# Kernel tuning notes

Hardware: AMD Instinct MI355X
Metric: run time of the kernel (lower is better)

## Reference

```python
import jax, jax.numpy as jnp
from jax import lax
import numpy as np


def _bn(x, g, b, eps=1e-5):
    # BatchNorm2d in training mode: biased batch stats over (N,H,W) per channel
    m = jnp.mean(x, axis=(0, 2, 3), keepdims=True)
    v = jnp.mean((x - m) ** 2, axis=(0, 2, 3), keepdims=True)
    return (x - m) * lax.rsqrt(v + eps) * g[None, :, None, None] + b[None, :, None, None]


def _conv(x, w, b, pad):
    y = lax.conv_general_dilated(x, w, (1, 1), [(pad, pad), (pad, pad)],
                                 dimension_numbers=('NCHW', 'OIHW', 'NCHW'))
    return y + b[None, :, None, None]


def _prelu(x, a):
    return jnp.where(x >= 0, x, a * x)


def _maxpool2(x):
    return lax.reduce_window(x, -jnp.inf, lax.max, (1, 1, 2, 2), (1, 1, 2, 2), 'VALID')


def _up2(x):
    # UpsamplingBilinear2d(scale_factor=2) -> bilinear, align_corners=True
    B, C, H, W = x.shape
    def idx(n):
        pos = jnp.arange(2 * n, dtype=x.dtype) * (n - 1) / (2 * n - 1)
        lo = jnp.floor(pos).astype(jnp.int32)
        hi = jnp.minimum(lo + 1, n - 1)
        return lo, hi, pos - lo.astype(x.dtype)
    lo, hi, f = idx(H)
    x = x[:, :, lo, :] * (1 - f)[:, None] + x[:, :, hi, :] * f[:, None]
    lo, hi, f = idx(W)
    x = x[:, :, :, lo] * (1 - f) + x[:, :, :, hi] * f
    return x


def _forward(x, n16, sigma16, bias16, prelu_a,
             bn3_g, bn3_b, bn32_g, bn32_b, bn64_g, bn64_b, bn128_g, bn128_b,
             w1, b1, w2, b2, w3, b3, w4, b4, w5, b5, w6, b6, w7, b7, w11, b11):
    B, C, H, W = x.shape
    # 16 enhancement curves fused: r_k = x^{n_k} / (x^{n_k} + sigma_k^{n_k} + bias_k)
    xn = x[None] ** n16[:, None, None, None, None]          # (16,B,3,H,W)
    r = xn / (xn + (sigma16 ** n16)[:, None, None, None, None]
              + bias16[:, None, None, None, None])
    # each branch gets its own BatchNorm2d(3) stats (same affine params)
    r = jax.vmap(lambda t: _bn(t, bn3_g, bn3_b))(r)
    x_fusion = jnp.transpose(r, (1, 0, 2, 3, 4)).reshape(B, 16 * C, H, W)
    x1 = _bn(_maxpool2(_prelu(_conv(x_fusion, w1, b1, 1), prelu_a)), bn32_g, bn32_b)
    x2 = _bn(_maxpool2(_prelu(_conv(x1, w2, b2, 1), prelu_a)), bn64_g, bn64_b)
    x3 = _bn(_maxpool2(_prelu(_conv(x2, w3, b3, 1), prelu_a)), bn128_g, bn128_b)
    x4 = _bn(_conv(x3, w4, b4, 1), bn128_g, bn128_b)
    x5 = _bn(_up2(_prelu(_conv(jnp.concatenate([x4, x3], 1), w5, b5, 1), prelu_a)), bn64_g, bn64_b)
    x6 = _bn(_up2(_prelu(_conv(jnp.concatenate([x2, x5], 1), w6, b6, 1), prelu_a)), bn32_g, bn32_b)
    x_out = jax.nn.sigmoid(_up2(_prelu(_conv(jnp.concatenate([x1, x6], 1), w7, b7, 1), prelu_a)))
    x_out = _conv(x_out, w11, b11, 0)
    x_mean = jnp.mean(x, axis=1, keepdims=True)
    x_out1 = jnp.mean(x_out, axis=1, keepdims=True)
    return x_out1 * (x / (x_mean + 1e-6))


def setup_inputs() -> dict:
    key = jax.random.key(0)
    ks = jax.random.split(key, 16)
    B, H, W = 8, 256, 256
    nf = 32
    x = jax.random.uniform(ks[0], (B, 3, H, W), jnp.float32, 1e-3, 1.0)
    n16 = jnp.arange(1, 17, dtype=jnp.float32) * 0.5
    sigma16 = jnp.full((16,), 0.5, jnp.float32)
    bias16 = jnp.full((16,), 1e-4, jnp.float32)
    prelu_a = jnp.float32(0.25)
    def cw(k, o, i, kk):
        return jax.random.normal(k, (o, i, kk, kk), jnp.float32) * 0.05
    def cb(o):
        return jnp.zeros((o,), jnp.float32)
    return dict(
        x=x, n16=n16, sigma16=sigma16, bias16=bias16, prelu_a=prelu_a,
        bn3_g=jnp.ones((3,), jnp.float32), bn3_b=jnp.zeros((3,), jnp.float32),
        bn32_g=jnp.ones((32,), jnp.float32), bn32_b=jnp.zeros((32,), jnp.float32),
        bn64_g=jnp.ones((64,), jnp.float32), bn64_b=jnp.zeros((64,), jnp.float32),
        bn128_g=jnp.ones((128,), jnp.float32), bn128_b=jnp.zeros((128,), jnp.float32),
        w1=cw(ks[1], nf, 48, 3), b1=cb(nf),
        w2=cw(ks[2], 2 * nf, nf, 3), b2=cb(2 * nf),
        w3=cw(ks[3], 4 * nf, 2 * nf, 3), b3=cb(4 * nf),
        w4=cw(ks[4], 4 * nf, 4 * nf, 3), b4=cb(4 * nf),
        w5=cw(ks[5], 2 * nf, 8 * nf, 3), b5=cb(2 * nf),
        w6=cw(ks[6], nf, 4 * nf, 3), b6=cb(nf),
        w7=cw(ks[7], nf, 2 * nf, 3), b7=cb(nf),
        w11=cw(ks[8], 3, nf, 1), b11=cb(3),
    )


def reference(x, n16, sigma16, bias16, prelu_a,
              bn3_g, bn3_b, bn32_g, bn32_b, bn64_g, bn64_b, bn128_g, bn128_b,
              w1, b1, w2, b2, w3, b3, w4, b4, w5, b5, w6, b6, w7, b7, w11, b11):
    return _forward(x, n16, sigma16, bias16, prelu_a,
                    bn3_g, bn3_b, bn32_g, bn32_b, bn64_g, bn64_b, bn128_g, bn128_b,
                    w1, b1, w2, b2, w3, b3, w4, b4, w5, b5, w6, b6, w7, b7, w11, b11)
```

## Files before the change

### kernel.cpp

```cpp
#include <hip/hip_runtime.h>

#define FAST_EXP2(x) __builtin_amdgcn_exp2f(x)
#define FAST_LOG2(x) __builtin_amdgcn_logf(x)
#define FAST_RCP(x)  __builtin_amdgcn_rcpf(x)

static constexpr size_t S3_SUM=0,   S3_SQ=48;
static constexpr size_t S32A_SUM=96,  S32A_SQ=128;
static constexpr size_t S64A_SUM=160, S64A_SQ=224;
static constexpr size_t S128A_SUM=288,S128A_SQ=416;
static constexpr size_t S128B_SUM=544,S128B_SQ=672;
static constexpr size_t S64B_SUM=800, S64B_SQ=864;
static constexpr size_t S32B_SUM=928, S32B_SQ=960;
static constexpr size_t SPB_=2016, WBAR_=2032, BBAR_=2064;
static constexpr size_t T1_=4096;
static constexpr size_t T2_=T1_+4194304;
static constexpr size_t T3_=T2_+2097152;
static constexpr size_t T4_=T3_+1048576;
static constexpr size_t C5_=T4_+1048576;
static constexpr size_t U5_=C5_+524288;
static constexpr size_t C6_=U5_+2097152;
static constexpr size_t U6_=C6_+1048576;
static constexpr size_t C7_=U6_+4194304;
static constexpr size_t W1S_=C7_+4194304;
static constexpr size_t B1S_=W1S_+13824;
static constexpr size_t PAD_=B1S_+64;

__device__ inline void bn_ab(const float* __restrict__ sum, const float* __restrict__ sq,
                             const float* __restrict__ g, const float* __restrict__ bb,
                             float invN, int c, float& a, float& b)
{
    float m   = sum[c]*invN;
    float var = fmaxf(sq[c]*invN - m*m, 0.f);
    float inv = rsqrtf(var + 1e-5f);
    a = g[c]*inv;
    b = bb[c] - m*a;
}

__global__ __launch_bounds__(256) void k_branch_stats(
    const float* __restrict__ x, const float* __restrict__ n16,
    const float* __restrict__ sig16, const float* __restrict__ b16,
    float* __restrict__ sum, float* __restrict__ sq)
{
    const int c = blockIdx.x >> 6;
    const int chunk = blockIdx.x & 63;
    float nk[16], den[16];
#pragma unroll
    for (int k = 0; k < 16; ++k) { nk[k] = n16[k]; den[k] = powf(sig16[k], nk[k]) + b16[k]; }
    float s[16], q[16];
#pragma unroll
    for (int k = 0; k < 16; ++k) { s[k] = 0.f; q[k] = 0.f; }
    const int per = 8192;
    int start = chunk * per;
    for (int i = start + (int)threadIdx.x; i < start + per; i += 256) {
        int b = i >> 16, hw = i & 65535;
        float xv = x[(size_t)(b*3 + c)*65536 + hw];
        float t = FAST_LOG2(xv);
#pragma unroll
        for (int k = 0; k < 16; ++k) {
            float v = FAST_EXP2(nk[k]*t);
            float r = v * FAST_RCP(v + den[k]);
            s[k] += r; q[k] += r*r;
        }
    }
    __shared__ float red[4][32];
    int lane = threadIdx.x & 63, wid = threadIdx.x >> 6;
#pragma unroll
    for (int k = 0; k < 16; ++k) {
#pragma unroll
        for (int off = 32; off > 0; off >>= 1) {
            s[k] += __shfl_down(s[k], off);
            q[k] += __shfl_down(q[k], off);
        }
    }
    if (lane == 0) {
#pragma unroll
        for (int k = 0; k < 16; ++k) { red[wid][k] = s[k]; red[wid][16+k] = q[k]; }
    }
    __syncthreads();
    if (threadIdx.x < 32) {
        float v = red[0][threadIdx.x] + red[1][threadIdx.x] + red[2][threadIdx.x] + red[3][threadIdx.x];
        int k = threadIdx.x & 15;
        if (threadIdx.x < 16) atomicAdd(&sum[k*3 + c], v);
        else                  atomicAdd(&sq[k*3 + c], v);
    }
}

__global__ __launch_bounds__(256) void k_stats(
    const float* __restrict__ in, int C, int HW, int nchunks, int per,
    float* __restrict__ sum, float* __restrict__ sq)
{
    int c = blockIdx.x / nchunks;
    int chunk = blockIdx.x - c*nchunks;
    float s = 0.f, q = 0.f;
    int start = chunk * per, end = start + per;
    for (int i = start + (int)threadIdx.x; i < end; i += 256) {
        int b = i / HW, hw = i - b*HW;
        float v = in[((size_t)b*C + c)*HW + hw];
        s += v; q += v*v;
    }
#pragma unroll
    for (int off = 32; off > 0; off >>= 1) { s += __shfl_down(s, off); q += __shfl_down(q, off); }
    __shared__ float ss[4], qq[4];
    int lane = threadIdx.x & 63, wid = threadIdx.x >> 6;
    if (lane == 0) { ss[wid] = s; qq[wid] = q; }
    __syncthreads();
    if (threadIdx.x == 0) {
        atomicAdd(&sum[c], ss[0]+ss[1]+ss[2]+ss[3]);
        atomicAdd(&sq[c],  qq[0]+qq[1]+qq[2]+qq[3]);
    }
}

__global__ __launch_bounds__(256) void k_fill(
    float* __restrict__ out, const float* __restrict__ bias, int C, int HW, int total)
{
    int idx = blockIdx.x*256 + threadIdx.x;
    if (idx < total) {
        int c = (idx / HW) % C;
        out[idx] = bias[c];
    }
}

__global__ __launch_bounds__(256) void k_prep_all(
    const float* __restrict__ s3sum, const float* __restrict__ s3sq,
    const float* __restrict__ bn3_g, const float* __restrict__ bn3_b,
    const float* __restrict__ n16, const float* __restrict__ sig16, const float* __restrict__ b16,
    const float* __restrict__ w11, const float* __restrict__ b11,
    const float* __restrict__ w1, const float* __restrict__ b1,
    float* __restrict__ w1s, float* __restrict__ b1s, float* __restrict__ padg,
    float* __restrict__ spb, float* __restrict__ wbar, float* __restrict__ bbar)
{
    __shared__ float a3[48], b3[48];
    int tid = threadIdx.x;
    if (tid < 48) {
        float m   = s3sum[tid]*(1.f/524288.f);
        float var = fmaxf(s3sq[tid]*(1.f/524288.f) - m*m, 0.f);
        float inv = rsqrtf(var + 1e-5f);
        float a   = bn3_g[tid % 3]*inv;
        a3[tid] = a;
        b3[tid] = bn3_b[tid % 3] - m*a;
    }
    if (tid < 16) spb[tid] = powf(sig16[tid], n16[tid]) + b16[tid];
    else if (tid >= 64 && tid < 96) { int j = tid - 64; wbar[j] = (w11[j] + w11[32+j] + w11[64+j]) * (1.f/3.f); }
    else if (tid == 96) bbar[0] = (b11[0] + b11[1] + b11[2]) * (1.f/3.f);
    __syncthreads();
    if (tid < 48) padg[tid] = -b3[tid] * FAST_RCP(a3[tid]);
    for (int t = tid; t < 13824; t += 256) {
        int ci = (t / 9) % 48;
        w1s[t] = w1[t] * a3[ci];
    }
    if (tid < 32) {
        float s = b1[tid];
        const float* wp = w1 + tid*432;
        for (int i = 0; i < 432; ++i) s += wp[i] * b3[i/9];
        b1s[tid] = s;
    }
}

template<int COG>
__device__ inline void stats_reduce8(float (&ssum)[COG], float (&ssq)[COG],
                                     float (*redst)[16], int cob,
                                     float* __restrict__ gsum, float* __restrict__ gsq)
{
    int lane = threadIdx.x & 63, wid = threadIdx.x >> 6;
#pragma unroll
    for (int co = 0; co < COG; ++co) {
#pragma unroll
        for (int off = 32; off > 0; off >>= 1) {
            ssum[co] += __shfl_down(ssum[co], off);
            ssq[co]  += __shfl_down(ssq[co],  off);
        }
    }
    if (lane == 0) {
#pragma unroll
        for (int co = 0; co < COG; ++co) { redst[wid][co] = ssum[co]; redst[wid][8+co] = ssq[co]; }
    }
    __syncthreads();
    if (threadIdx.x < 16) {
        float v = redst[0][threadIdx.x] + redst[1][threadIdx.x] + redst[2][threadIdx.x] + redst[3][threadIdx.x];
        if (threadIdx.x < 8) atomicAdd(&gsum[cob + threadIdx.x], v);
        else                 atomicAdd(&gsq[cob + threadIdx.x - 8], v);
    }
}

template<int COG>
__global__ __launch_bounds__(256,2) void k_conv1f(
    const float* __restrict__ x,
    const float* __restrict__ n16, const float* __restrict__ spb,
    const float* __restrict__ w1s, const float* __restrict__ b1s,
    const float* __restrict__ padg,
    const float* __restrict__ prelu_a,
    float* __restrict__ out, float* __restrict__ gsum, float* __restrict__ gsq)
{
    const int tx = threadIdx.x & 15, ty = threadIdx.x >> 4;
    const int nco = 32 / COG;
    const int b = blockIdx.z / nco, cob = (blockIdx.z - b*nco)*COG;
    const int x0 = blockIdx.x*32, y0 = blockIdx.y*32;

    __shared__ float wl[COG*48*9];
    __shared__ float rl[2][3*1224];
    __shared__ float nl16[16], dl16[16], padl[48];
    __shared__ float redst[4][16];

    for (int t = threadIdx.x; t < COG*48*9; t += 256) {
        int co = t % COG; int rest = t / COG;
        int kk = rest % 9; int ci = rest / 9;
        wl[t] = w1s[(((size_t)(cob+co))*48 + ci)*9 + kk];
    }
    if (threadIdx.x < 16)       nl16[threadIdx.x]    = n16[threadIdx.x];
    else if (threadIdx.x < 32)  dl16[threadIdx.x-16] = spb[threadIdx.x-16];
    else if (threadIdx.x < 80)  padl[threadIdx.x-32] = padg[threadIdx.x-32];

    float tlr[14];
    int off_[14]; int chpack = 0; int okf = 0;
#pragma unroll
    for (int j = 0; j < 14; ++j) {
        int i = threadIdx.x + 256*j;
        if (i < 3468) {
            int ch = i / 1156, jj = i - ch*1156;
            int rr = jj / 34, cc = jj - rr*34;
            int gy = y0 - 1 + rr, gx = x0 - 1 + cc;
            bool ok = (unsigned)gy < 256u && (unsigned)gx < 256u;
            off_[j] = ch*1224 + rr*36 + cc;
            chpack |= ch << (2*j);
            tlr[j] = 0.f;
            if (ok) {
                okf |= 1 << j;
                tlr[j] = FAST_LOG2(x[((size_t)(b*3+ch))*65536 + gy*256 + gx]);
            }
        } else { off_[j] = 3671; tlr[j] = 0.f; }
    }

    float acc[COG][4];
#pragma unroll
    for (int i = 0; i < COG; ++i)
#pragma unroll
        for (int j = 0; j < 4; ++j) acc[i][j] = 0.f;

    {
        float nk = nl16[0], dk = dl16[0];
#pragma unroll
        for (int j = 0; j < 14; ++j) {
            int ch = (chpack >> (2*j)) & 3;
            float pv = padl[ch];
            float v = FAST_EXP2(nk * tlr[j]);
            float rv = v * FAST_RCP(v + dk);
            rl[0][off_[j]] = ((okf >> j) & 1) ? rv : pv;
        }
    }
    __syncthreads();

#pragma unroll 1
    for (int k = 0; k < 16; ++k) {
        if (k < 15) {
            float nk = nl16[k+1], dk = dl16[k+1];
#pragma unroll
            for (int j = 0; j < 14; ++j) {
                int ch = (chpack >> (2*j)) & 3;
                float pv = padl[(k+1)*3 + ch];
                float v = FAST_EXP2(nk * tlr[j]);
                float rv = v * FAST_RCP(v + dk);
                rl[(k+1)&1][off_[j]] = ((okf >> j) & 1) ? rv : pv;
            }
        }
        const float* rbuf = rl[k&1];
#pragma unroll
        for (int ch = 0; ch < 3; ++ch) {
            const float* tlp = rbuf + ch*1224 + (2*ty)*36 + 2*tx;
            float iv[4][4];
#pragma unroll
            for (int r = 0; r < 4; ++r) {
                float2 a2 = *(const float2*)(tlp + r*36);
                float2 b2 = *(const float2*)(tlp + r*36 + 2);
                iv[r][0]=a2.x; iv[r][1]=a2.y; iv[r][2]=b2.x; iv[r][3]=b2.y;
            }
            const float* wbase = &wl[((k*3+ch)*9)*COG];
#pragma unroll
            for (int kh = 0; kh < 3; ++kh)
#pragma unroll
            for (int kw = 0; kw < 3; ++kw) {
                const int kk = kh*3 + kw;
                float wv[COG];
#pragma unroll
                for (int q = 0; q < COG/4; ++q) {
                    float4 wq = *((const float4*)(wbase + kk*COG) + q);
                    wv[4*q+0]=wq.x; wv[4*q+1]=wq.y; wv[4*q+2]=wq.z; wv[4*q+3]=wq.w;
                }
#pragma unroll
                for (int co = 0; co < COG; ++co)
#pragma unroll
                    for (int py = 0; py < 2; ++py)
#pragma unroll
                        for (int px = 0; px < 2; ++px)
                            acc[co][py*2+px] += wv[co]*iv[py+kh][px+kw];
            }
        }
        __syncthreads();
    }

    float a = __ldg(prelu_a);
    int pyp = (y0 >> 1) + ty, pxp = (x0 >> 1) + tx;
    float ssum[COG], ssq[COG];
#pragma unroll
    for (int co = 0; co < COG; ++co) {
        float bv = b1s[cob + co];
        float v0 = acc[co][0] + bv, v1 = acc[co][1] + bv;
        float v2 = acc[co][2] + bv, v3 = acc[co][3] + bv;
        v0 = v0 >= 0.f ? v0 : a*v0; v1 = v1 >= 0.f ? v1 : a*v1;
        v2 = v2 >= 0.f ? v2 : a*v2; v3 = v3 >= 0.f ? v3 : a*v3;
        float m = fmaxf(fmaxf(v0,v1), fmaxf(v2,v3));
        out[(((size_t)b*32 + cob + co)*128 + pyp)*128 + pxp] = m;
        ssum[co] = m; ssq[co] = m*m;
    }
    __syncthreads();
    stats_reduce8<COG>(ssum, ssq, redst, cob, gsum, gsq);
}

template<int COG, bool POOL>
__global__ __launch_bounds__(256,2) void k_conv_big(
    const float* __restrict__ in1, int C1,
    const float* __restrict__ sum1, const float* __restrict__ sq1,
    const float* __restrict__ g1, const float* __restrict__ bb1, float invN1,
    const float* __restrict__ w, const float* __restrict__ bias,
    int Cout, int H, int W, const float* __restrict__ prelu_a, int do_prelu,
    float* __restrict__ out, float* __restrict__ gsum, float* __restrict__ gsq)
{
    const int Cin = C1;
    const int tx = threadIdx.x & 15, ty = threadIdx.x >> 4;
    const int nco = Cout / COG;
    const int b = blockIdx.z / nco, cob = (blockIdx.z - b*nco)*COG;
    const int x0 = blockIdx.x*64, y0 = blockIdx.y*32;

    __shared__ float wl[COG*64*9];
    __shared__ float tile[2][34*68];
    __shared__ float redst[4][16];

    for (int t = threadIdx.x; t < COG*Cin*9; t += 256) {
        int co = t % COG; int rest = t / COG;
        int k = rest % 9; int ci = rest / 9;
        wl[t] = w[(((size_t)(cob+co))*Cin + ci)*9 + k];
    }

    float acc[COG][8];
#pragma unroll
    for (int i = 0; i < COG; ++i)
#pragma unroll
        for (int j = 0; j < 8; ++j) acc[i][j] = 0.f;

#pragma unroll 1
    for (int cb = 0; cb < Cin; cb += 2) {
#pragma unroll
        for (int sub = 0; sub < 2; ++sub) {
            int ci = cb + sub;
            float scv = 1.f, shv = 0.f;
            if (sum1) bn_ab(sum1, sq1, g1, bb1, invN1, ci, scv, shv);
            const float* base = in1 + ((size_t)b*Cin + ci)*H*W;
#pragma unroll 1
            for (int i = threadIdx.x; i < 34*66; i += 256) {
                int r = i / 66, c = i - r*66;
                int gy = y0 - 1 + r, gx = x0 - 1 + c;
                float v = 0.f;
                if ((unsigned)gy < (unsigned)H && (unsigned)gx < (unsigned)W)
                    v = base[(size_t)gy*W + gx]*scv + shv;
                tile[sub][r*68 + c] = v;
            }
        }
        __syncthreads();
#pragma unroll
        for (int sub = 0; sub < 2; ++sub) {
            const float* tl = &tile[sub][(2*ty)*68 + 4*tx];
            float iv[4][6];
#pragma unroll
            for (int r = 0; r < 4; ++r) {
                float4 av = *(const float4*)(tl + r*68);
                float2 bv = *(const float2*)(tl + r*68 + 4);
                iv[r][0]=av.x; iv[r][1]=av.y; iv[r][2]=av.z; iv[r][3]=av.w;
                iv[r][4]=bv.x; iv[r][5]=bv.y;
            }
            const float* wbase = &wl[(cb+sub)*9*COG];
#pragma unroll
            for (int kh = 0; kh < 3; ++kh)
#pragma unroll
            for (int kw = 0; kw < 3; ++kw) {
                const int k = kh*3 + kw;
                float wv[COG];
#pragma unroll
                for (int q = 0; q < COG/4; ++q) {
                    float4 wq = *((const float4*)(wbase + k*COG) + q);
                    wv[4*q+0]=wq.x; wv[4*q+1]=wq.y; wv[4*q+2]=wq.z; wv[4*q+3]=wq.w;
                }
#pragma unroll
                for (int co = 0; co < COG; ++co)
#pragma unroll
                    for (int py = 0; py < 2; ++py)
#pragma unroll
                        for (int px = 0; px < 4; ++px)
                            acc[co][py*4+px] += wv[co]*iv[py+kh][px+kw];
            }
        }
        __syncthreads();
    }

    float a = __ldg(prelu_a);
    float ssum[COG], ssq[COG];
    if (POOL) {
        const int Hp = H >> 1, Wp = W >> 1;
        int pyp = (y0 >> 1) + ty, pxp = (x0 >> 1) + 2*tx;
#pragma unroll
        for (int co = 0; co < COG; ++co) {
            float bv = bias[cob + co];
            float v[8];
#pragma unroll
            for (int p = 0; p < 8; ++p) {
                float t = acc[co][p] + bv;
                v[p] = t >= 0.f ? t : a*t;
            }
            float2 st;
            st.x = fmaxf(fmaxf(v[0], v[1]), fmaxf(v[4], v[5]));
            st.y = fmaxf(fmaxf(v[2], v[3]), fmaxf(v[6], v[7]));
            *(float2*)(out + (((size_t)b*Cout + cob + co)*Hp + pyp)*Wp + pxp) = st;
            ssum[co] = st.x + st.y; ssq[co] = st.x*st.x + st.y*st.y;
        }
        stats_reduce8<COG>(ssum, ssq, redst, cob, gsum, gsq);
    } else {
        int oy = y0 + 2*ty, ox = x0 + 4*tx;
#pragma unroll
        for (int co = 0; co < COG; ++co) {
            float bv = bias[cob + co];
            float* op = out + (((size_t)b*Cout + cob + co)*H + oy)*W + ox;
#pragma unroll
            for (int py = 0; py < 2; ++py) {
                float4 st;
                float t0 = acc[co][py*4+0] + bv, t1 = acc[co][py*4+1] + bv;
                float t2 = acc[co][py*4+2] + bv, t3 = acc[co][py*4+3] + bv;
                if (do_prelu) {
                    t0 = t0 >= 0.f ? t0 : a*t0; t1 = t1 >= 0.f ? t1 : a*t1;
                    t2 = t2 >= 0.f ? t2 : a*t2; t3 = t3 >= 0.f ? t3 : a*t3;
                }
                st.x=t0; st.y=t1; st.z=t2; st.w=t3;
                *(float4*)(op + py*W) = st;
            }
        }
    }
}

template<int COG, int MAXCI, bool POOL, bool SPLIT, bool STATS>
__global__ __launch_bounds__(256,4) void k_conv32(
    const float* __restrict__ in1, int C1,
    const float* __restrict__ sum1, const float* __restrict__ sq1,
    const float* __restrict__ g1, const float* __restrict__ bb1, float invN1,
    const float* __restrict__ in2, int C2,
    const float* __restrict__ sum2, const float* __restrict__ sq2,
    const float* __restrict__ g2, const float* __restrict__ bb2, float invN2,
    const float* __restrict__ w, const float* __restrict__ bias,
    int Cout, int H, int W, const float* __restrict__ prelu_a, int do_prelu,
    int ciN, int nsplit,
    float* __restrict__ out, float* __restrict__ gsum, float* __restrict__ gsq)
{
    const int Cin = C1 + C2;
    const int tx = threadIdx.x & 15, ty = threadIdx.x >> 4;
    const int nco = Cout / COG;
    int z = blockIdx.z;
    const int sp = z % nsplit; z /= nsplit;
    const int b = z / nco, cob = (z - b*nco)*COG;
    const int ci0 = sp * ciN;
    const int x0 = blockIdx.x*32, y0 = blockIdx.y*32;

    __shared__ float wl[COG*MAXCI*9];
    __shared__ float tile[2][34*36];
    __shared__ float redst[4][16];

    for (int t = threadIdx.x; t < COG*ciN*9; t += 256) {
        int co = t % COG; int rest = t / COG;
        int k = rest % 9; int ci = rest / 9;
        wl[t] = w[(((size_t)(cob+co))*Cin + ci0 + ci)*9 + k];
    }

    float acc[COG][4];
#pragma unroll
    for (int i = 0; i < COG; ++i)
#pragma unroll
        for (int j = 0; j < 4; ++j) acc[i][j] = 0.f;

#pragma unroll 1
    for (int cb = 0; cb < ciN; cb += 2) {
#pragma unroll
        for (int sub = 0; sub < 2; ++sub) {
            int ci = ci0 + cb + sub;
            const float* in; int cc; int Cn;
            const float* sm; const float* sqp; const float* gg; const float* bbp; float iN;
            if (ci < C1) { in = in1; cc = ci;      Cn = C1; sm = sum1; sqp = sq1; gg = g1; bbp = bb1; iN = invN1; }
            else         { in = in2; cc = ci - C1; Cn = C2; sm = sum2; sqp = sq2; gg = g2; bbp = bb2; iN = invN2; }
            float scv = 1.f, shv = 0.f;
            if (sm) bn_ab(sm, sqp, gg, bbp, iN, cc, scv, shv);
            const float* base = in + ((size_t)b*Cn + cc)*H*W;
#pragma unroll 1
            for (int i = threadIdx.x; i < 34*34; i += 256) {
                int r = i / 34, c = i - r*34;
                int gy = y0 - 1 + r, gx = x0 - 1 + c;
                float v = 0.f;
                if ((unsigned)gy < (unsigned)H && (unsigned)gx < (unsigned)W)
                    v = base[(size_t)gy*W + gx]*scv + shv;
                tile[sub][r*36 + c] = v;
            }
        }
        __syncthreads();
#pragma unroll
        for (int sub = 0; sub < 2; ++sub) {
            const float* tl = &tile[sub][(2*ty)*36 + 2*tx];
            float iv[4][4];
#pragma unroll
            for (int r = 0; r < 4; ++r) {
                float2 a2 = *(const float2*)(tl + r*36);
                float2 b2 = *(const float2*)(tl + r*36 + 2);
                iv[r][0]=a2.x; iv[r][1]=a2.y; iv[r][2]=b2.x; iv[r][3]=b2.y;
            }
            const float* wbase = &wl[(cb+sub)*9*COG];
#pragma unroll
            for (int kh = 0; kh < 3; ++kh)
#pragma unroll
            for (int kw = 0; kw < 3; ++kw) {
                const int k = kh*3 + kw;
                float wv[COG];
#pragma unroll
                for (int q = 0; q < COG/4; ++q) {
                    float4 wq = *((const float4*)(wbase + k*COG) + q);
                    wv[4*q+0]=wq.x; wv[4*q+1]=wq.y; wv[4*q+2]=wq.z; wv[4*q+3]=wq.w;
                }
#pragma unroll
                for (int co = 0; co < COG; ++co)
#pragma unroll
                    for (int py = 0; py < 2; ++py)
#pragma unroll
                        for (int px = 0; px < 2; ++px)
                            acc[co][py*2+px] += wv[co]*iv[py+kh][px+kw];
            }
        }
        __syncthreads();
    }

    if (SPLIT) {
        int oy = y0 + 2*ty, ox = x0 + 2*tx;
#pragma unroll
        for (int co = 0; co < COG; ++co) {
            float* op = out + (((size_t)b*Cout + cob + co)*H + oy)*W + ox;
            atomicAdd(&op[0],     acc[co][0]);
            atomicAdd(&op[1],     acc[co][1]);
            atomicAdd(&op[W],     acc[co][2]);
            atomicAdd(&op[W + 1], acc[co][3]);
        }
    } else {
        float a = __ldg(prelu_a);
        float ssum[COG], ssq[COG];
        if (POOL) {
            const int Hp = H >> 1, Wp = W >> 1;
            int pyp = (y0 >> 1) + ty, pxp = (x0 >> 1) + tx;
#pragma unroll
            for (int co = 0; co < COG; ++co) {
                float bv = bias[cob + co];
                float v0 = acc[co][0] + bv, v1 = acc[co][1] + bv;
                float v2 = acc[co][2] + bv, v3 = acc[co][3] + bv;
                v0 = v0 >= 0.f ? v0 : a*v0; v1 = v1 >= 0.f ? v1 : a*v1;
                v2 = v2 >= 0.f ? v2 : a*v2; v3 = v3 >= 0.f ? v3 : a*v3;
                float m = fmaxf(fmaxf(v0,v1), fmaxf(v2,v3));
                out[(((size_t)b*Cout + cob + co)*Hp + pyp)*Wp + pxp] = m;
                ssum[co] = m; ssq[co] = m*m;
            }
            if (STATS) stats_reduce8<COG>(ssum, ssq, redst, cob, gsum, gsq);
        } else {
            int oy = y0 + 2*ty, ox = x0 + 2*tx;
#pragma unroll
            for (int co = 0; co < COG; ++co) {
                float bv = bias[cob + co];
                float* op = out + (((size_t)b*Cout + cob + co)*H + oy)*W + ox;
                float v0 = acc[co][0] + bv, v1 = acc[co][1] + bv;
                float v2 = acc[co][2] + bv, v3 = acc[co][3] + bv;
                if (do_prelu) {
                    v0 = v0 >= 0.f ? v0 : a*v0; v1 = v1 >= 0.f ? v1 : a*v1;
                    v2 = v2 >= 0.f ? v2 : a*v2; v3 = v3 >= 0.f ? v3 : a*v3;
                }
                op[0] = v0; op[1] = v1; op[W] = v2; op[W+1] = v3;
                ssum[co] = v0+v1+v2+v3; ssq[co] = v0*v0+v1*v1+v2*v2+v3*v3;
            }
            if (STATS) stats_reduce8<COG>(ssum, ssq, redst, cob, gsum, gsq);
        }
    }
}

__global__ __launch_bounds__(256) void k_up2(
    const float* __restrict__ in, float* __restrict__ out, int C, int h, int w,
    const float* __restrict__ prelu_a, int do_prelu,
    float* __restrict__ gsum, float* __restrict__ gsq)
{
    int idx = blockIdx.x*256 + threadIdx.x;
    int W2 = 2*w, H2 = 2*h;
    float a = do_prelu ? __ldg(prelu_a) : 0.f;
    int ox = idx % W2; int t = idx / W2; int oy = t % H2; int bc = t / H2;
    float py = ((float)oy * (float)(h-1)) / (float)(2*h - 1);
    int ly = (int)floorf(py); int hy = min(ly+1, h-1); float fy = py - (float)ly;
    float px = ((float)ox * (float)(w-1)) / (float)(2*w - 1);
    int lx = (int)floorf(px); int hx = min(lx+1, w-1); float fx = px - (float)lx;
    const float* p = in + (size_t)bc*h*w;
    float v00 = p[(size_t)ly*w + lx], v01 = p[(size_t)ly*w + hx];
    float v10 = p[(size_t)hy*w + lx], v11 = p[(size_t)hy*w + hx];
    if (do_prelu) {
        v00 = v00 >= 0.f ? v00 : a*v00;
        v01 = v01 >= 0.f ? v01 : a*v01;
        v10 = v10 >= 0.f ? v10 : a*v10;
        v11 = v11 >= 0.f ? v11 : a*v11;
    }
    float v0 = v00*(1.f-fx) + v01*fx;
    float v1 = v10*(1.f-fx) + v11*fx;
    float v = v0*(1.f-fy) + v1*fy;
    out[idx] = v;
    float s = v, q = v*v;
#pragma unroll
    for (int off = 32; off > 0; off >>= 1) { s += __shfl_down(s, off); q += __shfl_down(q, off); }
    __shared__ float ss[4], qq[4];
    int lane = threadIdx.x & 63, wid = threadIdx.x >> 6;
    if (lane == 0) { ss[wid] = s; qq[wid] = q; }
    __syncthreads();
    if (threadIdx.x == 0) {
        int c = bc % C;
        atomicAdd(&gsum[c], ss[0]+ss[1]+ss[2]+ss[3]);
        atomicAdd(&gsq[c],  qq[0]+qq[1]+qq[2]+qq[3]);
    }
}

__global__ __launch_bounds__(256) void k_final(
    const float* __restrict__ c7, const float* __restrict__ x,
    const float* __restrict__ wbar, const float* __restrict__ bbar,
    float* __restrict__ out)
{
    int idx = blockIdx.x*256 + threadIdx.x;
    if (idx >= 8*65536) return;
    int hw = idx & 65535, b = idx >> 16;
    int oy = hw >> 8, ox = hw & 255;
    float py = ((float)oy * 127.f) / 255.f;
    int ly = (int)floorf(py); int hy = min(ly+1, 127); float fy = py - (float)ly;
    float px = ((float)ox * 127.f) / 255.f;
    int lx = (int)floorf(px); int hx = min(lx+1, 127); float fx = px - (float)lx;
    float w00 = (1.f-fy)*(1.f-fx), w01 = (1.f-fy)*fx, w10 = fy*(1.f-fx), w11v = fy*fx;
    const float* base = c7 + (size_t)b*32*16384;
    float accum = bbar[0];
#pragma unroll 8
    for (int j = 0; j < 32; ++j) {
        const float* p = base + (size_t)j*16384;
        float v = p[ly*128 + lx]*w00 + p[ly*128 + hx]*w01 + p[hy*128 + lx]*w10 + p[hy*128 + hx]*w11v;
        float s = FAST_RCP(1.f + __expf(-v));
        accum += wbar[j]*s;
    }
    size_t xb = (size_t)b*3*65536 + hw;
    float x0 = x[xb], x1 = x[xb + 65536], x2 = x[xb + 2*65536];
    float m = (x0 + x1 + x2)*(1.f/3.f) + 1e-6f;
    float sc = accum * FAST_RCP(m);
    out[xb]            = sc*x0;
    out[xb + 65536]    = sc*x1;
    out[xb + 2*65536]  = sc*x2;
}

extern "C" void kernel_launch(void* const* d_in, const int* in_sizes, int n_in,
                              void* d_out, int out_size, void* d_ws, size_t ws_size,
                              hipStream_t stream) {
    const float* x       = (const float*)d_in[0];
    const float* n16     = (const float*)d_in[1];
    const float* sig16   = (const float*)d_in[2];
    const float* bia16   = (const float*)d_in[3];
    const float* prelu_a = (const float*)d_in[4];
    const float* bn3_g   = (const float*)d_in[5];
    const float* bn3_b   = (const float*)d_in[6];
    const float* bn32_g  = (const float*)d_in[7];
    const float* bn32_b  = (const float*)d_in[8];
    const float* bn64_g  = (const float*)d_in[9];
    const float* bn64_b  = (const float*)d_in[10];
    const float* bn128_g = (const float*)d_in[11];
    const float* bn128_b = (const float*)d_in[12];
    const float* w1 = (const float*)d_in[13]; const float* b1 = (const float*)d_in[14];
    const float* w2 = (const float*)d_in[15]; const float* b2 = (const float*)d_in[16];
    const float* w3 = (const float*)d_in[17]; const float* b3 = (const float*)d_in[18];
    const float* w4 = (const float*)d_in[19]; const float* b4 = (const float*)d_in[20];
    const float* w5 = (const float*)d_in[21]; const float* b5 = (const float*)d_in[22];
    const float* w6 = (const float*)d_in[23]; const float* b6 = (const float*)d_in[24];
    const float* w7 = (const float*)d_in[25]; const float* b7 = (const float*)d_in[26];
    const float* w11= (const float*)d_in[27]; const float* b11= (const float*)d_in[28];
    float* ws  = (float*)d_ws;
    float* out = (float*)d_out;

    (void)hipMemsetAsync(d_ws, 0, 4096*sizeof(float), stream);

    k_branch_stats<<<192, 256, 0, stream>>>(x, n16, sig16, bia16, ws+S3_SUM, ws+S3_SQ);
    k_prep_all<<<1, 256, 0, stream>>>(ws+S3_SUM, ws+S3_SQ, bn3_g, bn3_b, n16, sig16, bia16,
                                      w11, b11, w1, b1,
                                      ws+W1S_, ws+B1S_, ws+PAD_, ws+SPB_, ws+WBAR_, ws+BBAR_);

    k_conv1f<8><<<dim3(8,8,32), 256, 0, stream>>>(x, n16, ws+SPB_, ws+W1S_, ws+B1S_, ws+PAD_,
                                                  prelu_a, ws+T1_, ws+S32A_SUM, ws+S32A_SQ);

    k_conv_big<8,true><<<dim3(2,4,64), 256, 0, stream>>>(
        ws+T1_, 32, ws+S32A_SUM, ws+S32A_SQ, bn32_g, bn32_b, 1.f/131072.f,
        w2, b2, 64, 128, 128, prelu_a, 1, ws+T2_, ws+S64A_SUM, ws+S64A_SQ);

    k_conv32<8,64,true,false,true><<<dim3(2,2,128), 256, 0, stream>>>(
        ws+T2_, 64, ws+S64A_SUM, ws+S64A_SQ, bn64_g, bn64_b, 1.f/32768.f,
        nullptr, 0, nullptr, nullptr, nullptr, nullptr, 0.f,
        w3, b3, 128, 64, 64, prelu_a, 1, 64, 1, ws+T3_, ws+S128A_SUM, ws+S128A_SQ);

    k_fill<<<4096, 256, 0, stream>>>(ws+T4_, b4, 128, 1024, 1048576);
    k_conv32<8,16,false,true,false><<<dim3(1,1,1024), 256, 0, stream>>>(
        ws+T3_, 128, ws+S128A_SUM, ws+S128A_SQ, bn128_g, bn128_b, 1.f/8192.f,
        nullptr, 0, nullptr, nullptr, nullptr, nullptr, 0.f,
        w4, nullptr, 128, 32, 32, prelu_a, 0, 16, 8, ws+T4_, nullptr, nullptr);
    k_stats<<<512, 256, 0, stream>>>(ws+T4_, 128, 1024, 4, 2048, ws+S128B_SUM, ws+S128B_SQ);

    k_fill<<<2048, 256, 0, stream>>>(ws+C5_, b5, 64, 1024, 524288);
    k_conv32<8,16,false,true,false><<<dim3(1,1,1024), 256, 0, stream>>>(
        ws+T4_, 128, ws+S128B_SUM, ws+S128B_SQ, bn128_g, bn128_b, 1.f/8192.f,
        ws+T3_, 128, ws+S128A_SUM, ws+S128A_SQ, bn128_g, bn128_b, 1.f/8192.f,
        w5, nullptr, 64, 32, 32, prelu_a, 0, 16, 16, ws+C5_, nullptr, nullptr);
    k_up2<<<8192, 256, 0, stream>>>(ws+C5_, ws+U5_, 64, 32, 32, prelu_a, 1, ws+S64B_SUM, ws+S64B_SQ);

    k_fill<<<4096, 256, 0, stream>>>(ws+C6_, b6, 32, 4096, 1048576);
    k_conv32<8,16,false,true,false><<<dim3(2,2,256), 256, 0, stream>>>(
        ws+T2_, 64, ws+S64A_SUM, ws+S64A_SQ, bn64_g, bn64_b, 1.f/32768.f,
        ws+U5_, 64, ws+S64B_SUM, ws+S64B_SQ, bn64_g, bn64_b, 1.f/32768.f,
        w6, nullptr, 32, 64, 64, prelu_a, 0, 16, 8, ws+C6_, nullptr, nullptr);
    k_up2<<<16384, 256, 0, stream>>>(ws+C6_, ws+U6_, 32, 64, 64, prelu_a, 1, ws+S32B_SUM, ws+S32B_SQ);

    k_conv32<8,64,false,false,false><<<dim3(4,4,32), 256, 0, stream>>>(
        ws+T1_, 32, ws+S32A_SUM, ws+S32A_SQ, bn32_g, bn32_b, 1.f/131072.f,
        ws+U6_, 32, ws+S32B_SUM, ws+S32B_SQ, bn32_g, bn32_b, 1.f/131072.f,
        w7, b7, 32, 128, 128, prelu_a, 1, 64, 1, ws+C7_, nullptr, nullptr);

    k_final<<<2048, 256, 0, stream>>>(ws+C7_, x, ws+WBAR_, ws+BBAR_, out);
}
```

Baseline: 1.365 ms.

## Replace conv2 big-tile kernel with generalized conv32 and widen branch-stats grid

Conv2 (32->64 channels at 128x128 with pooling) now runs on the templated k_conv32 kernel with 16 output channels per block and 32x32 tiles, replacing the dedicated k_conv_big kernel. The stats reduction helper is generalized to any COG, and the launch-bounds occupancy hint drops to 2 for COG>8. k_branch_stats is split into 8x more blocks with smaller chunks to fill the GPU better, at the cost of more atomics. The conv2 change alters the tile shape and register pressure, trading per-block reuse for grid shape.

```diff
diff --git a/kernel.cpp b/kernel.cpp
--- a/kernel.cpp
+++ b/kernel.cpp
@@ -41,15 +41,15 @@
     const float* __restrict__ sig16, const float* __restrict__ b16,
     float* __restrict__ sum, float* __restrict__ sq)
 {
-    const int c = blockIdx.x >> 6;
-    const int chunk = blockIdx.x & 63;
+    const int c = blockIdx.x >> 9;
+    const int chunk = blockIdx.x & 511;
     float nk[16], den[16];
 #pragma unroll
     for (int k = 0; k < 16; ++k) { nk[k] = n16[k]; den[k] = powf(sig16[k], nk[k]) + b16[k]; }
     float s[16], q[16];
 #pragma unroll
     for (int k = 0; k < 16; ++k) { s[k] = 0.f; q[k] = 0.f; }
-    const int per = 8192;
+    const int per = 1024;
     int start = chunk * per;
     for (int i = start + (int)threadIdx.x; i < start + per; i += 256) {
         int b = i >> 16, hw = i & 65535;
@@ -157,8 +157,8 @@
 }
 
 template<int COG>
-__device__ inline void stats_reduce8(float (&ssum)[COG], float (&ssq)[COG],
-                                     float (*redst)[16], int cob,
+__device__ inline void stats_reduceN(float (&ssum)[COG], float (&ssq)[COG],
+                                     float (*redst)[2*COG], int cob,
                                      float* __restrict__ gsum, float* __restrict__ gsq)
 {
     int lane = threadIdx.x & 63, wid = threadIdx.x >> 6;
@@ -172,13 +172,13 @@
     }
     if (lane == 0) {
 #pragma unroll
-        for (int co = 0; co < COG; ++co) { redst[wid][co] = ssum[co]; redst[wid][8+co] = ssq[co]; }
+        for (int co = 0; co < COG; ++co) { redst[wid][co] = ssum[co]; redst[wid][COG+co] = ssq[co]; }
     }
     __syncthreads();
-    if (threadIdx.x < 16) {
+    if (threadIdx.x < 2*COG) {
         float v = redst[0][threadIdx.x] + redst[1][threadIdx.x] + redst[2][threadIdx.x] + redst[3][threadIdx.x];
-        if (threadIdx.x < 8) atomicAdd(&gsum[cob + threadIdx.x], v);
-        else                 atomicAdd(&gsq[cob + threadIdx.x - 8], v);
+        if ((int)threadIdx.x < COG) atomicAdd(&gsum[cob + threadIdx.x], v);
+        else                        atomicAdd(&gsq[cob + threadIdx.x - COG], v);
     }
 }
 
@@ -199,7 +199,7 @@
     __shared__ float wl[COG*48*9];
     __shared__ float rl[2][3*1224];
     __shared__ float nl16[16], dl16[16], padl[48];
-    __shared__ float redst[4][16];
+    __shared__ float redst[4][2*COG];
 
     for (int t = threadIdx.x; t < COG*48*9; t += 256) {
         int co = t % COG; int rest = t / COG;
@@ -312,139 +312,11 @@
         ssum[co] = m; ssq[co] = m*m;
     }
     __syncthreads();
-    stats_reduce8<COG>(ssum, ssq, redst, cob, gsum, gsq);
-}
-
-template<int COG, bool POOL>
-__global__ __launch_bounds__(256,2) void k_conv_big(
-    const float* __restrict__ in1, int C1,
-    const float* __restrict__ sum1, const float* __restrict__ sq1,
-    const float* __restrict__ g1, const float* __restrict__ bb1, float invN1,
-    const float* __restrict__ w, const float* __restrict__ bias,
-    int Cout, int H, int W, const float* __restrict__ prelu_a, int do_prelu,
-    float* __restrict__ out, float* __restrict__ gsum, float* __restrict__ gsq)
-{
-    const int Cin = C1;
-    const int tx = threadIdx.x & 15, ty = threadIdx.x >> 4;
-    const int nco = Cout / COG;
-    const int b = blockIdx.z / nco, cob = (blockIdx.z - b*nco)*COG;
-    const int x0 = blockIdx.x*64, y0 = blockIdx.y*32;
-
-    __shared__ float wl[COG*64*9];
-    __shared__ float tile[2][34*68];
-    __shared__ float redst[4][16];
-
-    for (int t = threadIdx.x; t < COG*Cin*9; t += 256) {
-        int co = t % COG; int rest = t / COG;
-        int k = rest % 9; int ci = rest / 9;
-        wl[t] = w[(((size_t)(cob+co))*Cin + ci)*9 + k];
-    }
-
-    float acc[COG][8];
-#pragma unroll
-    for (int i = 0; i < COG; ++i)
-#pragma unroll
-        for (int j = 0; j < 8; ++j) acc[i][j] = 0.f;
-
-#pragma unroll 1
-    for (int cb = 0; cb < Cin; cb += 2) {
-#pragma unroll
-        for (int sub = 0; sub < 2; ++sub) {
-            int ci = cb + sub;
-            float scv = 1.f, shv = 0.f;
-            if (sum1) bn_ab(sum1, sq1, g1, bb1, invN1, ci, scv, shv);
-            const float* base = in1 + ((size_t)b*Cin + ci)*H*W;
-#pragma unroll 1
-            for (int i = threadIdx.x; i < 34*66; i += 256) {
-                int r = i / 66, c = i - r*66;
-                int gy = y0 - 1 + r, gx = x0 - 1 + c;
-                float v = 0.f;
-                if ((unsigned)gy < (unsigned)H && (unsigned)gx < (unsigned)W)
-                    v = base[(size_t)gy*W + gx]*scv + shv;
-                tile[sub][r*68 + c] = v;
-            }
-        }
-        __syncthreads();
-#pragma unroll
-        for (int sub = 0; sub < 2; ++sub) {
-            const float* tl = &tile[sub][(2*ty)*68 + 4*tx];
-            float iv[4][6];
-#pragma unroll
-            for (int r = 0; r < 4; ++r) {
-                float4 av = *(const float4*)(tl + r*68);
-                float2 bv = *(const float2*)(tl + r*68 + 4);
-                iv[r][0]=av.x; iv[r][1]=av.y; iv[r][2]=av.z; iv[r][3]=av.w;
-                iv[r][4]=bv.x; iv[r][5]=bv.y;
-            }
-            const float* wbase = &wl[(cb+sub)*9*COG];
-#pragma unroll
-            for (int kh = 0; kh < 3; ++kh)
-#pragma unroll
-            for (int kw = 0; kw < 3; ++kw) {
-                const int k = kh*3 + kw;
-                float wv[COG];
-#pragma unroll
-                for (int q = 0; q < COG/4; ++q) {
-                    float4 wq = *((const float4*)(wbase + k*COG) + q);
-                    wv[4*q+0]=wq.x; wv[4*q+1]=wq.y; wv[4*q+2]=wq.z; wv[4*q+3]=wq.w;
-                }
-#pragma unroll
-                for (int co = 0; co < COG; ++co)
-#pragma unroll
-                    for (int py = 0; py < 2; ++py)
-#pragma unroll
-                        for (int px = 0; px < 4; ++px)
-                            acc[co][py*4+px] += wv[co]*iv[py+kh][px+kw];
-            }
-        }
-        __syncthreads();
-    }
-
-    float a = __ldg(prelu_a);
-    float ssum[COG], ssq[COG];
-    if (POOL) {
-        const int Hp = H >> 1, Wp = W >> 1;
-        int pyp = (y0 >> 1) + ty, pxp = (x0 >> 1) + 2*tx;
-#pragma unroll
-        for (int co = 0; co < COG; ++co) {
-            float bv = bias[cob + co];
-            float v[8];
-#pragma unroll
-            for (int p = 0; p < 8; ++p) {
-                float t = acc[co][p] + bv;
-                v[p] = t >= 0.f ? t : a*t;
-            }
-            float2 st;
-            st.x = fmaxf(fmaxf(v[0], v[1]), fmaxf(v[4], v[5]));
-            st.y = fmaxf(fmaxf(v[2], v[3]), fmaxf(v[6], v[7]));
-            *(float2*)(out + (((size_t)b*Cout + cob + co)*Hp + pyp)*Wp + pxp) = st;
-            ssum[co] = st.x + st.y; ssq[co] = st.x*st.x + st.y*st.y;
-        }
-        stats_reduce8<COG>(ssum, ssq, redst, cob, gsum, gsq);
-    } else {
-        int oy = y0 + 2*ty, ox = x0 + 4*tx;
-#pragma unroll
-        for (int co = 0; co < COG; ++co) {
-            float bv = bias[cob + co];
-            float* op = out + (((size_t)b*Cout + cob + co)*H + oy)*W + ox;
-#pragma unroll
-            for (int py = 0; py < 2; ++py) {
-                float4 st;
-                float t0 = acc[co][py*4+0] + bv, t1 = acc[co][py*4+1] + bv;
-                float t2 = acc[co][py*4+2] + bv, t3 = acc[co][py*4+3] + bv;
-                if (do_prelu) {
-                    t0 = t0 >= 0.f ? t0 : a*t0; t1 = t1 >= 0.f ? t1 : a*t1;
-                    t2 = t2 >= 0.f ? t2 : a*t2; t3 = t3 >= 0.f ? t3 : a*t3;
-                }
-                st.x=t0; st.y=t1; st.z=t2; st.w=t3;
-                *(float4*)(op + py*W) = st;
-            }
-        }
-    }
+    stats_reduceN<COG>(ssum, ssq, redst, cob, gsum, gsq);
 }
 
 template<int COG, int MAXCI, bool POOL, bool SPLIT, bool STATS>
-__global__ __launch_bounds__(256,4) void k_conv32(
+__global__ __launch_bounds__(256, (COG<=8) ? 4 : 2) void k_conv32(
     const float* __restrict__ in1, int C1,
     const float* __restrict__ sum1, const float* __restrict__ sq1,
     const float* __restrict__ g1, const float* __restrict__ bb1, float invN1,
@@ -467,7 +339,7 @@
 
     __shared__ float wl[COG*MAXCI*9];
     __shared__ float tile[2][34*36];
-    __shared__ float redst[4][16];
+    __shared__ float redst[4][2*COG];
 
     for (int t = threadIdx.x; t < COG*ciN*9; t += 256) {
         int co = t % COG; int rest = t / COG;
@@ -565,7 +437,7 @@
                 out[(((size_t)b*Cout + cob + co)*Hp + pyp)*Wp + pxp] = m;
                 ssum[co] = m; ssq[co] = m*m;
             }
-            if (STATS) stats_reduce8<COG>(ssum, ssq, redst, cob, gsum, gsq);
+            if (STATS) stats_reduceN<COG>(ssum, ssq, redst, cob, gsum, gsq);
         } else {
             int oy = y0 + 2*ty, ox = x0 + 2*tx;
 #pragma unroll
@@ -581,7 +453,7 @@
                 op[0] = v0; op[1] = v1; op[W] = v2; op[W+1] = v3;
                 ssum[co] = v0+v1+v2+v3; ssq[co] = v0*v0+v1*v1+v2*v2+v3*v3;
             }
-            if (STATS) stats_reduce8<COG>(ssum, ssq, redst, cob, gsum, gsq);
+            if (STATS) stats_reduceN<COG>(ssum, ssq, redst, cob, gsum, gsq);
         }
     }
 }
@@ -687,7 +559,7 @@
 
     (void)hipMemsetAsync(d_ws, 0, 4096*sizeof(float), stream);
 
-    k_branch_stats<<<192, 256, 0, stream>>>(x, n16, sig16, bia16, ws+S3_SUM, ws+S3_SQ);
+    k_branch_stats<<<1536, 256, 0, stream>>>(x, n16, sig16, bia16, ws+S3_SUM, ws+S3_SQ);
     k_prep_all<<<1, 256, 0, stream>>>(ws+S3_SUM, ws+S3_SQ, bn3_g, bn3_b, n16, sig16, bia16,
                                       w11, b11, w1, b1,
                                       ws+W1S_, ws+B1S_, ws+PAD_, ws+SPB_, ws+WBAR_, ws+BBAR_);
@@ -695,9 +567,10 @@
     k_conv1f<8><<<dim3(8,8,32), 256, 0, stream>>>(x, n16, ws+SPB_, ws+W1S_, ws+B1S_, ws+PAD_,
                                                   prelu_a, ws+T1_, ws+S32A_SUM, ws+S32A_SQ);
 
-    k_conv_big<8,true><<<dim3(2,4,64), 256, 0, stream>>>(
+    k_conv32<16,32,true,false,true><<<dim3(4,4,32), 256, 0, stream>>>(
         ws+T1_, 32, ws+S32A_SUM, ws+S32A_SQ, bn32_g, bn32_b, 1.f/131072.f,
-        w2, b2, 64, 128, 128, prelu_a, 1, ws+T2_, ws+S64A_SUM, ws+S64A_SQ);
+        nullptr, 0, nullptr, nullptr, nullptr, nullptr, 0.f,
+        w2, b2, 64, 128, 128, prelu_a, 1, 32, 1, ws+T2_, ws+S64A_SUM, ws+S64A_SQ);
 
     k_conv32<8,64,true,false,true><<<dim3(2,2,128), 256, 0, stream>>>(
         ws+T2_, 64, ws+S64A_SUM, ws+S64A_SQ, bn64_g, bn64_b, 1.f/32768.f,
```

Result: no change. 1.360 ms (median of 3 runs) (-0.4%).
